# Kernel tuning notes

Hardware: AMD Instinct MI355X
Metric: run time of the kernel (lower is better)

## Reference

```python
import jax, jax.numpy as jnp
import numpy as np

N = 50000   # nodes (cells)
E = 800000  # directed edges
D = 512     # input/output feature dim (genes)
H = D // 64 # bottleneck dim = 8
LN_EPS = 1e-5


def setup_inputs() -> dict:
    key = jax.random.key(0)
    ks = jax.random.split(key, 6)
    x = jax.random.normal(ks[0], (N, D), dtype=jnp.float32)
    edge_index = jax.random.randint(ks[1], (2, E), 0, N, dtype=jnp.int64)
    size_factors = jax.random.uniform(ks[2], (N, 1), dtype=jnp.float32) + 0.5
    s1 = float(1.0 / np.sqrt(D))
    W1 = jax.random.uniform(ks[3], (D, H), jnp.float32, -s1, s1)
    b1 = jnp.zeros((H,), jnp.float32)
    gamma = jnp.ones((H,), jnp.float32)
    beta = jnp.zeros((H,), jnp.float32)
    s2 = float(1.0 / np.sqrt(H))
    W2 = jax.random.uniform(ks[4], (H, D), jnp.float32, -s2, s2)
    b2 = jnp.zeros((D,), jnp.float32)
    return {"x": x, "size_factors": size_factors, "W1": W1, "b1": b1,
            "gamma": gamma, "beta": beta, "W2": W2, "b2": b2,
            "edge_index": edge_index}


def _gcn_conv(x, W, b, src, dst, norm):
    # PyG GCNConv: linear transform, then sym-normalized scatter-add aggregation.
    h = x @ W                                   # [N, out]
    msg = h[src] * norm[:, None]                # [E+N, out] gather + scale
    out = jax.ops.segment_sum(msg, dst, num_segments=N)  # scatter-add
    return out + b


def reference(x, size_factors, W1, b1, gamma, beta, W2, b2, edge_index):
    loops = jnp.arange(N, dtype=edge_index.dtype)
    src = jnp.concatenate([edge_index[0], loops])  # add self-loops
    dst = jnp.concatenate([edge_index[1], loops])
    deg = jax.ops.segment_sum(jnp.ones_like(src, dtype=x.dtype), dst,
                              num_segments=N)       # deg >= 1 via self-loops
    dinv = jax.lax.rsqrt(deg)
    norm = dinv[src] * dinv[dst]                    # [E+N]

    h = _gcn_conv(x, W1, b1, src, dst, norm)        # [N, H]
    mu = jnp.mean(h, axis=-1, keepdims=True)
    var = jnp.var(h, axis=-1, keepdims=True)
    h = (h - mu) * jax.lax.rsqrt(var + LN_EPS) * gamma + beta
    h = jax.nn.relu(h)
    # dropout p=0.0 -> identity
    out = jax.nn.relu(_gcn_conv(h, W2, b2, src, dst, norm))  # [N, D]
    return out * size_factors
```

## Files before the change

### kernel.cpp

```cpp
#include <hip/hip_runtime.h>

#define NN 50000
#define EE 800000
#define DD 512
#define HH 8
#define SLOTS 64
#define GBLK 782
#define EBLK 3125
#define NTILE 3125
#define AGBLK 1563

typedef short bf16x8 __attribute__((ext_vector_type(8)));
typedef float f32x4 __attribute__((ext_vector_type(4)));

union U16 { uint4 u; bf16x8 v; unsigned short h[8]; };

__device__ __forceinline__ unsigned short f2bf(float f) {
    union { float f; unsigned int i; } c; c.f = f;
    unsigned int i = c.i;
    i += 0x7fffu + ((i >> 16) & 1u);
    return (unsigned short)(i >> 16);
}

__global__ __launch_bounds__(256) void k_fill_gemm1(const int* __restrict__ eidx,
                                                    const float4* __restrict__ x4,
                                                    const float* __restrict__ W1,
                                                    int* __restrict__ cur,
                                                    int* __restrict__ slots,
                                                    float* __restrict__ t1) {
    if (blockIdx.x >= GBLK) {
        int e = (blockIdx.x - GBLK) * 256 + threadIdx.x;
        if (e < EE) {
            int s = eidx[e], d = eidx[EE + e];
            int pos = atomicAdd(&cur[d], 1);
            if (pos < SLOTS) slots[(size_t)pos * NN + d] = s;
        }
        return;
    }
    __shared__ unsigned short sbf[16 * 64 * 8];
    for (int i = threadIdx.x; i < 16 * 64 * 8; i += 256) {
        int lane = (i >> 3) & 63, j = i & 7;
        int n = lane & 15;
        int k = (i >> 9) * 32 + ((lane >> 4) * 8) + j;
        sbf[i] = (n < HH) ? f2bf(W1[k * HH + n]) : (unsigned short)0;
    }
    __syncthreads();
    int wave = threadIdx.x >> 6, lane = threadIdx.x & 63;
    int tile = blockIdx.x * 4 + wave;
    if (tile >= NTILE) return;
    int node0 = tile * 16;
    int m = lane & 15, q = lane >> 4;
    const float4* xrow = x4 + (size_t)(node0 + m) * (DD / 4) + q * 2;
    const uint4* bfrag = (const uint4*)sbf;
    f32x4 acc = {0.f, 0.f, 0.f, 0.f};
#pragma unroll
    for (int step = 0; step < 16; ++step) {
        float4 u0 = xrow[step * 8];
        float4 u1 = xrow[step * 8 + 1];
        U16 a, b;
        a.h[0] = f2bf(u0.x); a.h[1] = f2bf(u0.y); a.h[2] = f2bf(u0.z); a.h[3] = f2bf(u0.w);
        a.h[4] = f2bf(u1.x); a.h[5] = f2bf(u1.y); a.h[6] = f2bf(u1.z); a.h[7] = f2bf(u1.w);
        b.u = bfrag[step * 64 + lane];
        acc = __builtin_amdgcn_mfma_f32_16x16x32_bf16(a.v, b.v, acc, 0, 0, 0);
    }
    if (m < HH) {
        int base = (node0 + q * 4) * HH + m;
        t1[base]          = acc[0];
        t1[base + HH]     = acc[1];
        t1[base + 2 * HH] = acc[2];
        t1[base + 3 * HH] = acc[3];
    }
}

__global__ __launch_bounds__(256) void k_agg1(const float* __restrict__ t1,
                                              const int* __restrict__ cur,
                                              const int* __restrict__ slots,
                                              const float* __restrict__ b1,
                                              const float* __restrict__ gma,
                                              const float* __restrict__ bta,
                                              float* __restrict__ h2) {
    int gid = blockIdx.x * 256 + threadIdx.x;
    int n = gid >> 3, f = gid & 7;
    if (n >= NN) return;
    int degr = cur[n];
    int deg = degr > SLOTS ? SLOTS : degr;
    float dv = rsqrtf((float)degr + 1.0f);
    float acc = t1[(size_t)n * HH + f] * dv;
    int i = 0;
    while (__ballot(i < deg)) {
        int  s0r = slots[(size_t)i * NN + n];
        int  s1r = slots[(size_t)(i + 1) * NN + n];
        bool v0 = i < deg, v1 = (i + 1) < deg;
        int  s0 = v0 ? s0r : 0, s1 = v1 ? s1r : 0;
        float w0 = v0 ? rsqrtf((float)cur[s0] + 1.0f) : 0.f;
        float w1 = v1 ? rsqrtf((float)cur[s1] + 1.0f) : 0.f;
        acc += t1[(size_t)s0 * HH + f] * w0;
        acc += t1[(size_t)s1 * HH + f] * w1;
        i += 2;
    }
    acc = acc * dv + b1[f];
    float s = acc;
    s += __shfl_xor(s, 1); s += __shfl_xor(s, 2); s += __shfl_xor(s, 4);
    float mu = s * 0.125f;
    float dx = acc - mu;
    float sq = dx * dx;
    sq += __shfl_xor(sq, 1); sq += __shfl_xor(sq, 2); sq += __shfl_xor(sq, 4);
    float var = sq * 0.125f;
    float rs = rsqrtf(var + 1e-5f);
    h2[(size_t)n * HH + f] = fmaxf(dx * rs * gma[f] + bta[f], 0.f);
}

__global__ __launch_bounds__(256) void k_agg2_gemm2(const float* __restrict__ h2,
                                                    const int* __restrict__ cur,
                                                    const int* __restrict__ slots,
                                                    const float* __restrict__ W2,
                                                    const float* __restrict__ b2,
                                                    const float* __restrict__ sf,
                                                    float* __restrict__ out) {
    __shared__ float sA[32 * 8];
    int tid = threadIdx.x;
    int c = tid & 63, g = tid >> 6, d0 = c * 8;
    float w[8][8];
#pragma unroll
    for (int k = 0; k < 8; ++k) {
        float4 u0 = *(const float4*)(W2 + k * DD + d0);
        float4 u1 = *(const float4*)(W2 + k * DD + d0 + 4);
        w[k][0] = u0.x; w[k][1] = u0.y; w[k][2] = u0.z; w[k][3] = u0.w;
        w[k][4] = u1.x; w[k][5] = u1.y; w[k][6] = u1.z; w[k][7] = u1.w;
    }
    float bb[8];
    {
        float4 u0 = *(const float4*)(b2 + d0);
        float4 u1 = *(const float4*)(b2 + d0 + 4);
        bb[0] = u0.x; bb[1] = u0.y; bb[2] = u0.z; bb[3] = u0.w;
        bb[4] = u1.x; bb[5] = u1.y; bb[6] = u1.z; bb[7] = u1.w;
    }
    int nl = tid >> 3, f = tid & 7;
    int n = blockIdx.x * 32 + nl;
    if (n < NN) {
        int degr = cur[n];
        int deg = degr > SLOTS ? SLOTS : degr;
        float dv = rsqrtf((float)degr + 1.0f);
        float acc = h2[(size_t)n * HH + f] * dv;
        int i = 0;
        while (__ballot(i < deg)) {
            int  s0r = slots[(size_t)i * NN + n];
            int  s1r = slots[(size_t)(i + 1) * NN + n];
            bool v0 = i < deg, v1 = (i + 1) < deg;
            int  s0 = v0 ? s0r : 0, s1 = v1 ? s1r : 0;
            float w0 = v0 ? rsqrtf((float)cur[s0] + 1.0f) : 0.f;
            float w1 = v1 ? rsqrtf((float)cur[s1] + 1.0f) : 0.f;
            acc += h2[(size_t)s0 * HH + f] * w0;
            acc += h2[(size_t)s1 * HH + f] * w1;
            i += 2;
        }
        sA[nl * 8 + f] = acc * dv;
    }
    __syncthreads();
#pragma unroll
    for (int i = 0; i < 8; ++i) {
        int row = i * 4 + g;
        int n2 = blockIdx.x * 32 + row;
        if (n2 < NN) {
            float a[8];
#pragma unroll
            for (int j = 0; j < 8; ++j) a[j] = sA[row * 8 + j];
            float s = sf[n2];
            float acc[8];
#pragma unroll
            for (int j = 0; j < 8; ++j) acc[j] = bb[j];
#pragma unroll
            for (int k = 0; k < 8; ++k)
#pragma unroll
                for (int j = 0; j < 8; ++j) acc[j] += a[k] * w[k][j];
            float4 o0 = make_float4(fmaxf(acc[0], 0.f) * s, fmaxf(acc[1], 0.f) * s,
                                    fmaxf(acc[2], 0.f) * s, fmaxf(acc[3], 0.f) * s);
            float4 o1 = make_float4(fmaxf(acc[4], 0.f) * s, fmaxf(acc[5], 0.f) * s,
                                    fmaxf(acc[6], 0.f) * s, fmaxf(acc[7], 0.f) * s);
            float4* op = (float4*)(out + (size_t)n2 * DD + d0);
            op[0] = o0;
            op[1] = o1;
        }
    }
}

extern "C" void kernel_launch(void* const* d_in, const int* in_sizes, int n_in,
                              void* d_out, int out_size, void* d_ws, size_t ws_size,
                              hipStream_t stream) {
    (void)in_sizes; (void)n_in; (void)out_size; (void)ws_size;
    const float* x   = (const float*)d_in[0];
    const float* sf  = (const float*)d_in[1];
    const float* W1  = (const float*)d_in[2];
    const float* b1  = (const float*)d_in[3];
    const float* gma = (const float*)d_in[4];
    const float* bta = (const float*)d_in[5];
    const float* W2  = (const float*)d_in[6];
    const float* b2  = (const float*)d_in[7];
    const int* eidx  = (const int*)d_in[8];
    float* out = (float*)d_out;

    char* ws = (char*)d_ws;
    int*   cur   = (int*)(ws + 0);
    int*   slots = (int*)(ws + (1 << 20));
    float* t1    = (float*)(ws + 16 * (1 << 20));
    float* h2    = (float*)(ws + 18 * (1 << 20));

    hipMemsetAsync(cur, 0, NN * sizeof(int), stream);
    k_fill_gemm1<<<GBLK + EBLK, 256, 0, stream>>>(eidx, (const float4*)x, W1,
                                                  cur, slots, t1);
    k_agg1<<<AGBLK, 256, 0, stream>>>(t1, cur, slots, b1, gma, bta, h2);
    k_agg2_gemm2<<<AGBLK, 256, 0, stream>>>(h2, cur, slots, W2, b2, sf, out);
}
```

Before: 297.8 us.

## Replace atomic slot-table adjacency with two-level binned CSR build

Swaps the per-destination global-atomic slot table (capped at 64 neighbours, column-major layout) for a CSR built in stages: a block-local histogram by 256-node bin, a scan, a scatter into bins, and a per-bin LDS counting sort that emits row offsets, adjacency and precomputed inverse-sqrt degree. The aggregation kernels then walk contiguous CSR ranges and read the precomputed dinv instead of recomputing rsqrt from counts. This is meant to cut contended global atomics and scattered slot reads. It adds three small kernel launches plus a serial single-block scan. It also silently caps each bin at BCAP edges.

```diff
diff --git a/kernel.cpp b/kernel.cpp
--- a/kernel.cpp
+++ b/kernel.cpp
@@ -4,9 +4,11 @@
 #define EE 800000
 #define DD 512
 #define HH 8
-#define SLOTS 64
+#define BA 160
+#define CHUNK 5000
+#define NBIN 196
+#define BCAP 4608
 #define GBLK 782
-#define EBLK 3125
 #define NTILE 3125
 #define AGBLK 1563
 
@@ -22,59 +24,158 @@
     return (unsigned short)(i >> 16);
 }
 
-__global__ __launch_bounds__(256) void k_fill_gemm1(const int* __restrict__ eidx,
-                                                    const float4* __restrict__ x4,
-                                                    const float* __restrict__ W1,
-                                                    int* __restrict__ cur,
-                                                    int* __restrict__ slots,
-                                                    float* __restrict__ t1) {
-    if (blockIdx.x >= GBLK) {
-        int e = (blockIdx.x - GBLK) * 256 + threadIdx.x;
-        if (e < EE) {
-            int s = eidx[e], d = eidx[EE + e];
-            int pos = atomicAdd(&cur[d], 1);
-            if (pos < SLOTS) slots[(size_t)pos * NN + d] = s;
+__global__ __launch_bounds__(256) void k_hist(const int* __restrict__ dst,
+                                              int* __restrict__ blockhist) {
+    __shared__ int h[256];
+    int t = threadIdx.x, blk = blockIdx.x;
+    h[t] = 0; __syncthreads();
+    int base = blk * CHUNK;
+#pragma unroll
+    for (int it = 0; it < 20; ++it) {
+        int i = it * 256 + t;
+        if (i < CHUNK) atomicAdd(&h[dst[base + i] >> 8], 1);
+    }
+    __syncthreads();
+    blockhist[blk * 256 + t] = h[t];
+}
+
+__global__ __launch_bounds__(256) void k_scan(int* __restrict__ blockhist,
+                                              int* __restrict__ binBase,
+                                              int* __restrict__ row) {
+    __shared__ int s[256];
+    int t = threadIdx.x;
+    int sum = 0;
+    for (int b = 0; b < BA; ++b) sum += blockhist[b * 256 + t];
+    s[t] = sum; __syncthreads();
+    for (int off = 1; off < 256; off <<= 1) {
+        int x = (t >= off) ? s[t - off] : 0;
+        __syncthreads();
+        if (t >= off) s[t] += x;
+        __syncthreads();
+    }
+    int excl = s[t] - sum;
+    binBase[t] = excl;
+    if (t == 255) { binBase[256] = s[255]; row[NN] = s[255]; }
+    int run = excl;
+    for (int b = 0; b < BA; ++b) {
+        int v = blockhist[b * 256 + t];
+        blockhist[b * 256 + t] = run;
+        run += v;
+    }
+}
+
+__global__ __launch_bounds__(256) void k_scatter(const int* __restrict__ eidx,
+                                                 const int* __restrict__ blockhist,
+                                                 int2* __restrict__ bucket) {
+    __shared__ int cur[256];
+    int t = threadIdx.x, blk = blockIdx.x;
+    cur[t] = blockhist[blk * 256 + t]; __syncthreads();
+    int base = blk * CHUNK;
+#pragma unroll
+    for (int it = 0; it < 20; ++it) {
+        int i = it * 256 + t;
+        if (i < CHUNK) {
+            int s = eidx[base + i], d = eidx[EE + base + i];
+            int pos = atomicAdd(&cur[d >> 8], 1);
+            bucket[pos] = make_int2(s, d);
+        }
+    }
+}
+
+__global__ __launch_bounds__(256) void k_build_gemm1(const int2* __restrict__ bucket,
+                                                     const int* __restrict__ binBase,
+                                                     const float4* __restrict__ x4,
+                                                     const float* __restrict__ W1,
+                                                     int* __restrict__ row,
+                                                     int* __restrict__ adj,
+                                                     float* __restrict__ dinvA,
+                                                     float* __restrict__ t1) {
+    __shared__ int smem[11264];
+    int t = threadIdx.x;
+    if (blockIdx.x >= NBIN) {
+        unsigned short* sbf = (unsigned short*)smem;
+        for (int i = t; i < 16 * 64 * 8; i += 256) {
+            int lane = (i >> 3) & 63, j = i & 7;
+            int n = lane & 15;
+            int k = (i >> 9) * 32 + ((lane >> 4) * 8) + j;
+            sbf[i] = (n < HH) ? f2bf(W1[k * HH + n]) : (unsigned short)0;
+        }
+        __syncthreads();
+        int wave = t >> 6, lane = t & 63;
+        int tile = (blockIdx.x - NBIN) * 4 + wave;
+        if (tile >= NTILE) return;
+        int node0 = tile * 16;
+        int m = lane & 15, q = lane >> 4;
+        const float4* xrow = x4 + (size_t)(node0 + m) * (DD / 4) + q * 2;
+        const uint4* bfrag = (const uint4*)sbf;
+        f32x4 acc = {0.f, 0.f, 0.f, 0.f};
+#pragma unroll
+        for (int step = 0; step < 16; ++step) {
+            float4 u0 = xrow[step * 8];
+            float4 u1 = xrow[step * 8 + 1];
+            U16 a, b;
+            a.h[0] = f2bf(u0.x); a.h[1] = f2bf(u0.y); a.h[2] = f2bf(u0.z); a.h[3] = f2bf(u0.w);
+            a.h[4] = f2bf(u1.x); a.h[5] = f2bf(u1.y); a.h[6] = f2bf(u1.z); a.h[7] = f2bf(u1.w);
+            b.u = bfrag[step * 64 + lane];
+            acc = __builtin_amdgcn_mfma_f32_16x16x32_bf16(a.v, b.v, acc, 0, 0, 0);
+        }
+        if (m < HH) {
+            int base = (node0 + q * 4) * HH + m;
+            t1[base]          = acc[0];
+            t1[base + HH]     = acc[1];
+            t1[base + 2 * HH] = acc[2];
+            t1[base + 3 * HH] = acc[3];
         }
         return;
     }
-    __shared__ unsigned short sbf[16 * 64 * 8];
-    for (int i = threadIdx.x; i < 16 * 64 * 8; i += 256) {
-        int lane = (i >> 3) & 63, j = i & 7;
-        int n = lane & 15;
-        int k = (i >> 9) * 32 + ((lane >> 4) * 8) + j;
-        sbf[i] = (n < HH) ? f2bf(W1[k * HH + n]) : (unsigned short)0;
-    }
-    __syncthreads();
-    int wave = threadIdx.x >> 6, lane = threadIdx.x & 63;
-    int tile = blockIdx.x * 4 + wave;
-    if (tile >= NTILE) return;
-    int node0 = tile * 16;
-    int m = lane & 15, q = lane >> 4;
-    const float4* xrow = x4 + (size_t)(node0 + m) * (DD / 4) + q * 2;
-    const uint4* bfrag = (const uint4*)sbf;
-    f32x4 acc = {0.f, 0.f, 0.f, 0.f};
-#pragma unroll
-    for (int step = 0; step < 16; ++step) {
-        float4 u0 = xrow[step * 8];
-        float4 u1 = xrow[step * 8 + 1];
-        U16 a, b;
-        a.h[0] = f2bf(u0.x); a.h[1] = f2bf(u0.y); a.h[2] = f2bf(u0.z); a.h[3] = f2bf(u0.w);
-        a.h[4] = f2bf(u1.x); a.h[5] = f2bf(u1.y); a.h[6] = f2bf(u1.z); a.h[7] = f2bf(u1.w);
-        b.u = bfrag[step * 64 + lane];
-        acc = __builtin_amdgcn_mfma_f32_16x16x32_bf16(a.v, b.v, acc, 0, 0, 0);
-    }
-    if (m < HH) {
-        int base = (node0 + q * 4) * HH + m;
-        t1[base]          = acc[0];
-        t1[base + HH]     = acc[1];
-        t1[base + 2 * HH] = acc[2];
-        t1[base + 3 * HH] = acc[3];
-    }
+    int bin = blockIdx.x;
+    int n0 = bin << 8;
+    int segStart = binBase[bin];
+    int count = binBase[bin + 1] - segStart;
+    if (count > BCAP) count = BCAP;
+    int* lds_s   = smem;
+    int* lds_out = smem + BCAP;
+    int* cnt     = smem + 2 * BCAP;
+    int* off     = smem + 2 * BCAP + 256;
+    int* cur2    = smem + 2 * BCAP + 512;
+    unsigned char* lds_d = (unsigned char*)(smem + 2 * BCAP + 768);
+    cnt[t] = 0; __syncthreads();
+    for (int i = t; i < count; i += 256) {
+        int2 p = bucket[segStart + i];
+        lds_s[i] = p.x;
+        int dl = p.y - n0;
+        lds_d[i] = (unsigned char)dl;
+        atomicAdd(&cnt[dl], 1);
+    }
+    __syncthreads();
+    off[t] = cnt[t]; __syncthreads();
+    for (int o = 1; o < 256; o <<= 1) {
+        int x = (t >= o) ? off[t - o] : 0;
+        __syncthreads();
+        if (t >= o) off[t] += x;
+        __syncthreads();
+    }
+    int excl = off[t] - cnt[t];
+    cur2[t] = excl;
+    int n = n0 + t;
+    if (n < NN) {
+        row[n] = segStart + excl;
+        dinvA[n] = rsqrtf((float)cnt[t] + 1.0f);
+    }
+    __syncthreads();
+    for (int i = t; i < count; i += 256) {
+        int pos = atomicAdd(&cur2[lds_d[i]], 1);
+        lds_out[pos] = lds_s[i];
+    }
+    __syncthreads();
+    for (int i = t; i < count; i += 256)
+        adj[segStart + i] = lds_out[i];
 }
 
 __global__ __launch_bounds__(256) void k_agg1(const float* __restrict__ t1,
-                                              const int* __restrict__ cur,
-                                              const int* __restrict__ slots,
+                                              const int* __restrict__ row,
+                                              const int* __restrict__ adj,
+                                              const float* __restrict__ dinvA,
                                               const float* __restrict__ b1,
                                               const float* __restrict__ gma,
                                               const float* __restrict__ bta,
@@ -82,21 +183,19 @@
     int gid = blockIdx.x * 256 + threadIdx.x;
     int n = gid >> 3, f = gid & 7;
     if (n >= NN) return;
-    int degr = cur[n];
-    int deg = degr > SLOTS ? SLOTS : degr;
-    float dv = rsqrtf((float)degr + 1.0f);
+    int beg = row[n], end = row[n + 1];
+    float dv = dinvA[n];
     float acc = t1[(size_t)n * HH + f] * dv;
-    int i = 0;
-    while (__ballot(i < deg)) {
-        int  s0r = slots[(size_t)i * NN + n];
-        int  s1r = slots[(size_t)(i + 1) * NN + n];
-        bool v0 = i < deg, v1 = (i + 1) < deg;
-        int  s0 = v0 ? s0r : 0, s1 = v1 ? s1r : 0;
-        float w0 = v0 ? rsqrtf((float)cur[s0] + 1.0f) : 0.f;
-        float w1 = v1 ? rsqrtf((float)cur[s1] + 1.0f) : 0.f;
+    int i = beg;
+    for (; i + 2 <= end; i += 2) {
+        int s0 = adj[i], s1 = adj[i + 1];
+        float w0 = dinvA[s0], w1 = dinvA[s1];
         acc += t1[(size_t)s0 * HH + f] * w0;
         acc += t1[(size_t)s1 * HH + f] * w1;
-        i += 2;
+    }
+    if (i < end) {
+        int s0 = adj[i];
+        acc += t1[(size_t)s0 * HH + f] * dinvA[s0];
     }
     acc = acc * dv + b1[f];
     float s = acc;
@@ -105,14 +204,14 @@
     float dx = acc - mu;
     float sq = dx * dx;
     sq += __shfl_xor(sq, 1); sq += __shfl_xor(sq, 2); sq += __shfl_xor(sq, 4);
-    float var = sq * 0.125f;
-    float rs = rsqrtf(var + 1e-5f);
+    float rs = rsqrtf(sq * 0.125f + 1e-5f);
     h2[(size_t)n * HH + f] = fmaxf(dx * rs * gma[f] + bta[f], 0.f);
 }
 
 __global__ __launch_bounds__(256) void k_agg2_gemm2(const float* __restrict__ h2,
-                                                    const int* __restrict__ cur,
-                                                    const int* __restrict__ slots,
+                                                    const int* __restrict__ row,
+                                                    const int* __restrict__ adj,
+                                                    const float* __restrict__ dinvA,
                                                     const float* __restrict__ W2,
                                                     const float* __restrict__ b2,
                                                     const float* __restrict__ sf,
@@ -138,33 +237,31 @@
     int nl = tid >> 3, f = tid & 7;
     int n = blockIdx.x * 32 + nl;
     if (n < NN) {
-        int degr = cur[n];
-        int deg = degr > SLOTS ? SLOTS : degr;
-        float dv = rsqrtf((float)degr + 1.0f);
+        int beg = row[n], end = row[n + 1];
+        float dv = dinvA[n];
         float acc = h2[(size_t)n * HH + f] * dv;
-        int i = 0;
-        while (__ballot(i < deg)) {
-            int  s0r = slots[(size_t)i * NN + n];
-            int  s1r = slots[(size_t)(i + 1) * NN + n];
-            bool v0 = i < deg, v1 = (i + 1) < deg;
-            int  s0 = v0 ? s0r : 0, s1 = v1 ? s1r : 0;
-            float w0 = v0 ? rsqrtf((float)cur[s0] + 1.0f) : 0.f;
-            float w1 = v1 ? rsqrtf((float)cur[s1] + 1.0f) : 0.f;
+        int i = beg;
+        for (; i + 2 <= end; i += 2) {
+            int s0 = adj[i], s1 = adj[i + 1];
+            float w0 = dinvA[s0], w1 = dinvA[s1];
             acc += h2[(size_t)s0 * HH + f] * w0;
             acc += h2[(size_t)s1 * HH + f] * w1;
-            i += 2;
+        }
+        if (i < end) {
+            int s0 = adj[i];
+            acc += h2[(size_t)s0 * HH + f] * dinvA[s0];
         }
         sA[nl * 8 + f] = acc * dv;
     }
     __syncthreads();
 #pragma unroll
     for (int i = 0; i < 8; ++i) {
-        int row = i * 4 + g;
-        int n2 = blockIdx.x * 32 + row;
+        int rrow = i * 4 + g;
+        int n2 = blockIdx.x * 32 + rrow;
         if (n2 < NN) {
             float a[8];
 #pragma unroll
-            for (int j = 0; j < 8; ++j) a[j] = sA[row * 8 + j];
+            for (int j = 0; j < 8; ++j) a[j] = sA[rrow * 8 + j];
             float s = sf[n2];
             float acc[8];
 #pragma unroll
@@ -200,14 +297,20 @@
     float* out = (float*)d_out;
 
     char* ws = (char*)d_ws;
-    int*   cur   = (int*)(ws + 0);
-    int*   slots = (int*)(ws + (1 << 20));
-    float* t1    = (float*)(ws + 16 * (1 << 20));
-    float* h2    = (float*)(ws + 18 * (1 << 20));
-
-    hipMemsetAsync(cur, 0, NN * sizeof(int), stream);
-    k_fill_gemm1<<<GBLK + EBLK, 256, 0, stream>>>(eidx, (const float4*)x, W1,
-                                                  cur, slots, t1);
-    k_agg1<<<AGBLK, 256, 0, stream>>>(t1, cur, slots, b1, gma, bta, h2);
-    k_agg2_gemm2<<<AGBLK, 256, 0, stream>>>(h2, cur, slots, W2, b2, sf, out);
-}
+    int*   blockhist = (int*)(ws + 0);
+    int*   binBase   = (int*)(ws + 262144);
+    int*   row       = (int*)(ws + (1 << 20));
+    float* dinvA     = (float*)(ws + 2 * (1 << 20));
+    float* t1        = (float*)(ws + 3 * (1 << 20));
+    float* h2        = (float*)(ws + 5 * (1 << 20));
+    int*   adj       = (int*)(ws + 7 * (1 << 20));
+    int2*  bucket    = (int2*)(ws + 11 * (1 << 20));
+
+    k_hist<<<BA, 256, 0, stream>>>(eidx + EE, blockhist);
+    k_scan<<<1, 256, 0, stream>>>(blockhist, binBase, row);
+    k_scatter<<<BA, 256, 0, stream>>>(eidx, blockhist, bucket);
+    k_build_gemm1<<<NBIN + GBLK, 256, 0, stream>>>(bucket, binBase, (const float4*)x,
+                                                   W1, row, adj, dinvA, t1);
+    k_agg1<<<AGBLK, 256, 0, stream>>>(t1, row, adj, dinvA, b1, gma, bta, h2);
+    k_agg2_gemm2<<<AGBLK, 256, 0, stream>>>(h2, row, adj, dinvA, W2, b2, sf, out);
+}
```

Result: faster. 285.2 us (-4.2%).
